# Kernel optimization log

Hardware: AMD Instinct MI355X
Metric: run time of the kernel (lower is better)

The kernel has to match this reference:

```python
import jax, jax.numpy as jnp
import numpy as np

B, T, D, DU, H = 2048, 100, 128, 128, 128  # batch, seq_len, emb_dim, user_emb_dim, hidden (=emb_dim)


def _mlp(x, layers, act):
    for W, b in layers:
        x = act(x @ W.T + b)
    return x


def setup_inputs() -> dict:
    key = jax.random.key(0)
    ks = iter(jax.random.split(key, 48))
    def p(shape, scale=0.05):
        return jax.random.normal(next(ks), shape, jnp.float32) * scale
    lengths = jax.random.randint(next(ks), (B,), 1, T + 1).astype(jnp.int32)
    mask = (jnp.arange(T)[None, :] < lengths[:, None]).astype(jnp.int32)
    inp = {
        'user_embedding': p((B, DU), 1.0),
        'item_historical_embedding': p((B, T, D), 1.0),
        'item_embedding': p((B, D), 1.0),
        'mask': mask,
        'sequential_length': lengths,
        'gru_Wih': p((3 * H, D)), 'gru_Whh': p((3 * H, H)),
        'gru_bih': p((3 * H,)), 'gru_bhh': p((3 * H,)),
        'aug_Wr': p((H, D + H)), 'aug_br': p((H,)),
        'aug_Wu': p((H, D + H)), 'aug_bu': p((H,)),
        'aug_Wh': p((H, D + H)), 'aug_bh': p((H,)),
    }
    att_dims = [4 * D, 80, 40, 1]
    ph_dims = [4 * D + DU, 200, 80, 1]
    for i, (di, do) in enumerate(zip(att_dims[:-1], att_dims[1:])):
        inp['att_W%d' % i] = p((do, di)); inp['att_b%d' % i] = p((do,))
    for i, (di, do) in enumerate(zip(ph_dims[:-1], ph_dims[1:])):
        inp['ph_W%d' % i] = p((do, di)); inp['ph_b%d' % i] = p((do,))
    return inp


def _forward(mask, sequential_length, user_embedding, item_historical_embedding, item_embedding,
             gru_Wih, gru_Whh, gru_bih, gru_bhh,
             att_W0, att_b0, att_W1, att_b1, att_W2, att_b2,
             aug_Wr, aug_br, aug_Wu, aug_bu, aug_Wh, aug_bh,
             ph_W0, ph_b0, ph_W1, ph_b1, ph_W2, ph_b2):
    fmask = mask.astype(jnp.float32)
    hist_sum = (item_historical_embedding * fmask[:, :, None]).sum(1)
    hist_sum = hist_sum / sequential_length[:, None].astype(jnp.float32)  # (B, D)

    # standard GRU over time (torch nn.GRU gate math) via lax.scan
    def gru_step(h, x_t):
        gi = x_t @ gru_Wih.T + gru_bih
        gh = h @ gru_Whh.T + gru_bhh
        i_r, i_z, i_n = jnp.split(gi, 3, axis=-1)
        h_r, h_z, h_n = jnp.split(gh, 3, axis=-1)
        r = jax.nn.sigmoid(i_r + h_r)
        z = jax.nn.sigmoid(i_z + h_z)
        n = jnp.tanh(i_n + r * h_n)
        h_new = (1.0 - z) * n + z * h
        return h_new, h_new
    h0 = jnp.zeros((item_historical_embedding.shape[0], H), jnp.float32)
    _, gru_seq = jax.lax.scan(gru_step, h0, jnp.swapaxes(item_historical_embedding, 0, 1))
    keys = jnp.swapaxes(gru_seq, 0, 1)  # (B, T, H)

    # DIN-style activation unit (all-ReLU MLP since act='relu'), masked softmax over time
    q = jnp.broadcast_to(item_embedding[:, None, :], keys.shape)
    feat = jnp.concatenate([keys, q, keys - q, q * keys], axis=-1)  # (B, T, 4H)
    score = _mlp(feat, [(att_W0, att_b0), (att_W1, att_b1), (att_W2, att_b2)], jax.nn.relu)
    score = jnp.where(mask[:, :, None] == 1, score, -jnp.inf)
    attn = jax.nn.softmax(score, axis=1)[..., 0]  # (B, T)
    # return_score=False in source: pooled context vector is (mis)used as attention scores
    pooled = jnp.einsum('bt,btd->bd', attn, keys)  # (B, H)

    # AUGRU; source indexes pooled[:, t] as per-step attention score (requires T <= H)
    att_seq = pooled.T[:T]  # (T, B)
    def augru_step(h, inp):
        x_t, a_t = inp
        ti = jnp.concatenate([h, x_t], axis=-1)
        r = jax.nn.sigmoid(ti @ aug_Wr.T + aug_br)
        u = jax.nn.sigmoid(ti @ aug_Wu.T + aug_bu)
        h_hat = jnp.tanh(jnp.concatenate([h * r, x_t], axis=-1) @ aug_Wh.T + aug_bh)
        u = a_t[:, None] * u
        h_new = (1.0 - u) * h + u * h_hat
        return h_new, h_new
    _, aug_seq = jax.lax.scan(augru_step, h0, (jnp.swapaxes(keys, 0, 1), att_seq))
    aug_out = jnp.swapaxes(aug_seq, 0, 1)  # (B, T, H)

    idx = (sequential_length - 1).astype(jnp.int32)[:, None, None]
    attention_feature = jnp.take_along_axis(aug_out, idx, axis=1)[:, 0, :]  # (B, H)

    comb = jnp.concatenate([user_embedding, item_embedding, hist_sum,
                            item_embedding * hist_sum, attention_feature], axis=1)
    # PredictHead: all layers sigmoid (source's i != len(dims)-1 is always True)
    scores = _mlp(comb, [(ph_W0, ph_b0), (ph_W1, ph_b1), (ph_W2, ph_b2)], jax.nn.sigmoid)
    return scores[:, 0]


def reference(user_embedding, item_historical_embedding, item_embedding, mask, sequential_length,
              gru_Wih, gru_Whh, gru_bih, gru_bhh,
              att_W0, att_b0, att_W1, att_b1, att_W2, att_b2,
              aug_Wr, aug_br, aug_Wu, aug_bu, aug_Wh, aug_bh,
              ph_W0, ph_b0, ph_W1, ph_b1, ph_W2, ph_b2):
    return _forward(mask, sequential_length, user_embedding, item_historical_embedding, item_embedding,
                    gru_Wih, gru_Whh, gru_bih, gru_bhh,
                    att_W0, att_b0, att_W1, att_b1, att_W2, att_b2,
                    aug_Wr, aug_br, aug_Wu, aug_bu, aug_Wh, aug_bh,
                    ph_W0, ph_b0, ph_W1, ph_b1, ph_W2, ph_b2)
```

## Files before the change

kernel.cpp:

```cpp
#include <hip/hip_runtime.h>
#include <math.h>

#define BB 2048
#define TT 100
#define DD 128
#define HH 128

typedef __attribute__((ext_vector_type(8))) short bf16x8;
typedef __attribute__((ext_vector_type(4))) float f32x4;

__device__ __forceinline__ float sigm(float x) {
    return __builtin_amdgcn_rcpf(1.f + __expf(-x));
}
__device__ __forceinline__ float tanh_fast(float x) {
    x = fminf(fmaxf(x, -15.f), 15.f);
    float e = __expf(2.f * x);
    return (e - 1.f) * __builtin_amdgcn_rcpf(e + 1.f);
}
__device__ __forceinline__ short f2bf(float f) {
    union { float f; unsigned u; } v; v.f = f;
    unsigned r = v.u + 0x7FFF + ((v.u >> 16) & 1);
    return (short)(r >> 16);
}
__device__ __forceinline__ float bf2f(ushort u) {
    union { unsigned u; float f; } v; v.u = ((unsigned)u) << 16;
    return v.f;
}

#define RD_A(buf, kk) (*(const bf16x8*)((const char*)(buf) + arow * 256 + (((kk) * 64 + akg * 16) ^ ((arow & 7) << 4))))
#define ST_A(buf, row, c, val) (*(short*)((char*)(buf) + (row) * 256 + (((c) * 2) ^ (((row) & 7) << 4))) = (val))

__global__ void k_prep(const float* __restrict__ attW0,
                       float* __restrict__ Wk, float* __restrict__ Wd, float* __restrict__ WqmC) {
    int i = blockIdx.x * 256 + threadIdx.x;
    if (i < 128 * 80) {
        int d = i / 80, j = i - d * 80;
        Wk[i]   = attW0[j * 512 + d] + attW0[j * 512 + 256 + d];
        Wd[i]   = attW0[j * 512 + 384 + d];
        WqmC[i] = attW0[j * 512 + 128 + d] - attW0[j * 512 + 256 + d];
    }
}

__global__ void k_pack(const float* __restrict__ Wih, const float* __restrict__ Whh,
                       const float* __restrict__ Wr, const float* __restrict__ Wu, const float* __restrict__ Wh,
                       const float* __restrict__ attW1,
                       const float* __restrict__ phW0, const float* __restrict__ phW1,
                       ushort* __restrict__ Pgru, ushort* __restrict__ Pa1, ushort* __restrict__ Pa2,
                       ushort* __restrict__ W1bf, ushort* __restrict__ W0h, ushort* __restrict__ W1h) {
    int n = blockIdx.x * 256 + threadIdx.x;
    if (n < 98304) {
        int tile = n >> 11, kt = (n >> 9) & 3, li = (n >> 3) & 63, e = n & 7;
        int k = kt * 32 + (li >> 4) * 8 + e;
        float s;
        if (tile < 24) { int j = tile * 16 + (li & 15); s = Wih[j * 128 + k]; }
        else           { int j = (tile - 24) * 16 + (li & 15); s = Whh[j * 128 + k]; }
        Pgru[n] = (ushort)f2bf(s);
    }
    if (n < 65536) {
        int tile = n >> 12, kt = (n >> 9) & 7, li = (n >> 3) & 63, e = n & 7;
        int k = kt * 32 + (li >> 4) * 8 + e;
        int jj = tile * 16 + (li & 15);
        float s = (jj < 128) ? Wr[jj * 256 + k] : Wu[(jj - 128) * 256 + k];
        Pa1[n] = (ushort)f2bf(s);
    }
    if (n < 32768) {
        int tile = n >> 12, kt = (n >> 9) & 7, li = (n >> 3) & 63, e = n & 7;
        int k = kt * 32 + (li >> 4) * 8 + e;
        int j = tile * 16 + (li & 15);
        Pa2[n] = (ushort)f2bf(Wh[j * 256 + k]);
    }
    if (n < 4608) {
        int g = n >> 9;
        int nt = g / 3, kt = g - nt * 3;
        int li = (n >> 3) & 63, e = n & 7;
        int k = kt * 32 + (li >> 4) * 8 + e;
        int j2 = nt * 16 + (li & 15);
        float s = (k < 80 && j2 < 40) ? attW1[j2 * 80 + k] : 0.f;
        W1bf[n] = (ushort)f2bf(s);
    }
    if (n < 133120) {
        int g = n >> 9;
        int nt = g / 20, kt = g - nt * 20;
        int li = (n >> 3) & 63, e = n & 7;
        int k = kt * 32 + (li >> 4) * 8 + e;
        int j = nt * 16 + (li & 15);
        W0h[n] = (ushort)f2bf((j < 200) ? phW0[j * 640 + k] : 0.f);
    }
    if (n < 17920) {
        int g = n >> 9;
        int nt = g / 7, kt = g - nt * 7;
        int li = (n >> 3) & 63, e = n & 7;
        int k = kt * 32 + (li >> 4) * 8 + e;
        int j = nt * 16 + (li & 15);
        W1h[n] = (ushort)f2bf((k < 200 && j < 80) ? phW1[j * 200 + k] : 0.f);
    }
}

__global__ void k_weffbf(const float* __restrict__ item, const float* __restrict__ Wk,
                         const float* __restrict__ Wd, const float* __restrict__ WqmC,
                         const float* __restrict__ attb0,
                         ushort* __restrict__ Weffbf, float* __restrict__ bias2) {
    int b = blockIdx.x, tid = threadIdx.x;
    __shared__ float q[128];
    if (tid < 128) q[tid] = item[b * 128 + tid];
    __syncthreads();
    ushort* Wb = Weffbf + (size_t)b * 10240;
    for (int idx = tid; idx < 10240; idx += 256) {
        int e = idx & 7, li = (idx >> 3) & 63, kt = (idx >> 9) & 3, nt = idx >> 11;
        int d = kt * 32 + (li >> 4) * 8 + e;
        int j = nt * 16 + (li & 15);
        Wb[idx] = (ushort)f2bf(Wk[d * 80 + j] + q[d] * Wd[d * 80 + j]);
    }
    if (tid < 80) {
        float s = attb0[tid];
        for (int d = 0; d < 128; ++d) s += q[d] * WqmC[d * 80 + tid];
        bias2[b * 80 + tid] = s;
    }
}

__global__ __launch_bounds__(512) void k_gru_mfma(const float* __restrict__ hist,
                                                  const ushort* __restrict__ Wp,
                                                  const float* __restrict__ bih, const float* __restrict__ bhh,
                                                  const int* __restrict__ len,
                                                  ushort* __restrict__ keysbf, float* __restrict__ hsum) {
    int tid = threadIdx.x;
    int lane = tid & 63, w = tid >> 6;
    int b0 = blockIdx.x * 8;

    __shared__ ushort xbf[2][16 * 128];
    __shared__ ushort hbf[2][16 * 128];
    __shared__ int    ln_s[8];

    for (int e = tid; e < 16 * 128; e += 512) { xbf[0][e] = 0; xbf[1][e] = 0; hbf[0][e] = 0; hbf[1][e] = 0; }
    if (tid < 8) ln_s[tid] = len[b0 + tid];

    const bf16x8* Wv = (const bf16x8*)Wp;
    bf16x8 bfx[3][4], bfh[3][4];
#pragma unroll
    for (int g = 0; g < 3; ++g)
#pragma unroll
        for (int kt = 0; kt < 4; ++kt) {
            bfx[g][kt] = Wv[((g * 8 + w) * 4 + kt) * 64 + lane];
            bfh[g][kt] = Wv[(((24 + g * 8 + w)) * 4 + kt) * 64 + lane];
        }

    int arow = lane & 15, akg = lane >> 4;
    int c = w * 16 + arow;
    float birq = bih[c] + bhh[c];
    float bizq = bih[128 + c] + bhh[128 + c];
    float bin  = bih[256 + c];
    float bqn  = bhh[256 + c];
    float hold[4] = {0.f, 0.f, 0.f, 0.f};

    int srow = tid >> 6, sd0 = (tid & 63) * 2;
    const float* hsrc = &hist[(size_t)(b0 + srow) * TT * DD + sd0];
    float2 v = *(const float2*)hsrc;
    __syncthreads();
    int Lrow = ln_s[srow];
    float sum0 = 0.f, sum1 = 0.f;
    {
        unsigned pv = (unsigned)(unsigned short)f2bf(v.x) | ((unsigned)(unsigned short)f2bf(v.y) << 16);
        *(unsigned*)((char*)xbf[0] + srow * 256 + ((sd0 * 2) ^ ((srow & 7) << 4))) = pv;
        if (0 < Lrow) { sum0 += v.x; sum1 += v.y; }
        if (TT > 1) v = *(const float2*)(hsrc + DD);
    }
    __syncthreads();

    f32x4 accr, accz, accnx;
    {
        bf16x8 af[4];
#pragma unroll
        for (int kt = 0; kt < 4; ++kt) af[kt] = RD_A(xbf[0], kt);
        accr = (f32x4){0.f,0.f,0.f,0.f}; accz = accr; accnx = accr;
#pragma unroll
        for (int kt = 0; kt < 4; ++kt) {
            accr  = __builtin_amdgcn_mfma_f32_16x16x32_bf16(af[kt], bfx[0][kt], accr, 0, 0, 0);
            accz  = __builtin_amdgcn_mfma_f32_16x16x32_bf16(af[kt], bfx[1][kt], accz, 0, 0, 0);
            accnx = __builtin_amdgcn_mfma_f32_16x16x32_bf16(af[kt], bfx[2][kt], accnx, 0, 0, 0);
        }
    }

    int p = 0, q = 0;
    for (int t = 0; t < TT; ++t) {
        if (t + 1 < TT) {
            unsigned pv = (unsigned)(unsigned short)f2bf(v.x) | ((unsigned)(unsigned short)f2bf(v.y) << 16);
            *(unsigned*)((char*)xbf[p ^ 1] + srow * 256 + ((sd0 * 2) ^ ((srow & 7) << 4))) = pv;
            if (t + 1 < Lrow) { sum0 += v.x; sum1 += v.y; }
            if (t + 2 < TT) v = *(const float2*)(hsrc + (size_t)(t + 2) * DD);
        }

        bf16x8 ah[4];
#pragma unroll
        for (int kt = 0; kt < 4; ++kt) ah[kt] = RD_A(hbf[q], kt);
        f32x4 accnh = {0.f, 0.f, 0.f, 0.f};
#pragma unroll
        for (int kt = 0; kt < 4; ++kt) {
            accr  = __builtin_amdgcn_mfma_f32_16x16x32_bf16(ah[kt], bfh[0][kt], accr, 0, 0, 0);
            accz  = __builtin_amdgcn_mfma_f32_16x16x32_bf16(ah[kt], bfh[1][kt], accz, 0, 0, 0);
            accnh = __builtin_amdgcn_mfma_f32_16x16x32_bf16(ah[kt], bfh[2][kt], accnh, 0, 0, 0);
        }

        ushort* hw = (ushort*)hbf[q ^ 1];
#pragma unroll
        for (int i = 0; i < 4; ++i) {
            float r = sigm(accr[i] + birq);
            float z = sigm(accz[i] + bizq);
            float nn = tanh_fast(accnx[i] + bin + r * (accnh[i] + bqn));
            float hnew = (1.f - z) * nn + z * hold[i];
            hold[i] = hnew;
            if (akg < 2) {
                int row = akg * 4 + i;
                short hb16 = f2bf(hnew);
                ST_A(hw, row, c, hb16);
                keysbf[((size_t)(b0 + row) * TT + t) * HH + c] = (ushort)hb16;
            }
        }
        __syncthreads();

        if (t + 1 < TT) {
            bf16x8 af[4];
#pragma unroll
            for (int kt = 0; kt < 4; ++kt) af[kt] = RD_A(xbf[p ^ 1], kt);
            f32x4 ar = {0.f,0.f,0.f,0.f}, az = ar, an = ar;
#pragma unroll
            for (int kt = 0; kt < 4; ++kt) {
                ar = __builtin_amdgcn_mfma_f32_16x16x32_bf16(af[kt], bfx[0][kt], ar, 0, 0, 0);
                az = __builtin_amdgcn_mfma_f32_16x16x32_bf16(af[kt], bfx[1][kt], az, 0, 0, 0);
                an = __builtin_amdgcn_mfma_f32_16x16x32_bf16(af[kt], bfx[2][kt], an, 0, 0, 0);
            }
            accr = ar; accz = az; accnx = an;
        }
        p ^= 1; q ^= 1;
    }

    hsum[(b0 + srow) * 128 + sd0]     = sum0 / (float)Lrow;
    hsum[(b0 + srow) * 128 + sd0 + 1] = sum1 / (float)Lrow;
}

__global__ __launch_bounds__(512) void k_attnsoft(const ushort* __restrict__ keysbf,
                                                  const ushort* __restrict__ Weffbf,
                                                  const float* __restrict__ bias2,
                                                  const ushort* __restrict__ W1bf,
                                                  const float* __restrict__ attb1, const float* __restrict__ attW2,
                                                  const float* __restrict__ attb2,
                                                  const int* __restrict__ len,
                                                  float* __restrict__ pooled) {
    int tid = threadIdx.x;
    int lane = tid & 63, w = tid >> 6;
    int b = blockIdx.x;

    __shared__ ushort kbf[112 * 128];
    __shared__ ushort scbf[112 * 96];
    __shared__ float  bias2s[80];
    __shared__ float  b1s[48];
    __shared__ float  W2s[48];
    __shared__ float  attn_s[128];
    __shared__ float  red[128];
    __shared__ float  pred[512];

    bf16x8 bfrag0[5][4];
    bf16x8 bfrag1[3][3];
    if (w < 7) {
        const bf16x8* Wb = (const bf16x8*)(Weffbf + (size_t)b * 10240);
#pragma unroll
        for (int nt = 0; nt < 5; ++nt)
#pragma unroll
            for (int kt = 0; kt < 4; ++kt)
                bfrag0[nt][kt] = Wb[(nt * 4 + kt) * 64 + lane];
#pragma unroll
        for (int nt = 0; nt < 3; ++nt)
#pragma unroll
            for (int kt = 0; kt < 3; ++kt)
                bfrag1[nt][kt] = ((const bf16x8*)W1bf)[(nt * 3 + kt) * 64 + lane];
    }

    const ushort* ksrc = keysbf + (size_t)b * TT * 128;
    for (int e = tid; e < 3584; e += 512) {
        int row = e >> 5, c4 = e & 31;
        uint2 pv;
        if (row < TT) pv = *(const uint2*)(ksrc + row * 128 + c4 * 4);
        else { pv.x = 0; pv.y = 0; }
        *(uint2*)((char*)kbf + row * 256 + ((c4 * 8) ^ ((row & 7) << 4))) = pv;
    }
    for (int e = tid; e < 1792; e += 512) {
        int row = e >> 4, c = 80 + (e & 15);
        *(ushort*)((char*)scbf + row * 192 + ((c * 2) ^ ((row & 7) << 4))) = 0;
    }
    if (tid < 80) bias2s[tid] = bias2[b * 80 + tid];
    if (tid < 48) {
        b1s[tid] = (tid < 40) ? attb1[tid] : 0.f;
        W2s[tid] = (tid < 40) ? attW2[tid] : 0.f;
    }
    __syncthreads();

    if (w < 7) {
        int arow = lane & 15, akg = lane >> 4;
        int row = w * 16 + arow;
        bf16x8 af[4];
#pragma unroll
        for (int kt = 0; kt < 4; ++kt)
            af[kt] = *(const bf16x8*)((const char*)kbf + row * 256 + (((kt * 64 + akg * 16)) ^ ((row & 7) << 4)));
#pragma unroll
        for (int nt = 0; nt < 5; ++nt) {
            f32x4 acc = {0.f, 0.f, 0.f, 0.f};
#pragma unroll
            for (int kt = 0; kt < 4; ++kt)
                acc = __builtin_amdgcn_mfma_f32_16x16x32_bf16(af[kt], bfrag0[nt][kt], acc, 0, 0, 0);
            int col = nt * 16 + arow;
            float bcol = bias2s[col];
#pragma unroll
            for (int i = 0; i < 4; ++i) {
                int r2 = w * 16 + akg * 4 + i;
                float vsc = fmaxf(acc[i] + bcol, 0.f);
                *(short*)((char*)scbf + r2 * 192 + ((col * 2) ^ ((r2 & 7) << 4))) = f2bf(vsc);
            }
        }
    }
    __syncthreads();

    if (w < 7) {
        int arow = lane & 15, akg = lane >> 4;
        int row = w * 16 + arow;
        bf16x8 a1[3];
#pragma unroll
        for (int kt = 0; kt < 3; ++kt)
            a1[kt] = *(const bf16x8*)((const char*)scbf + row * 192 + (((kt * 64 + akg * 16)) ^ ((row & 7) << 4)));
        float pi[4] = {0.f, 0.f, 0.f, 0.f};
#pragma unroll
        for (int nt = 0; nt < 3; ++nt) {
            f32x4 acc = {0.f, 0.f, 0.f, 0.f};
#pragma unroll
            for (int kt = 0; kt < 3; ++kt)
                acc = __builtin_amdgcn_mfma_f32_16x16x32_bf16(a1[kt], bfrag1[nt][kt], acc, 0, 0, 0);
            int col = nt * 16 + arow;
            float wb = W2s[col], bb1 = b1s[col];
#pragma unroll
            for (int i = 0; i < 4; ++i)
                pi[i] += fmaxf(acc[i] + bb1, 0.f) * wb;
        }
#pragma unroll
        for (int off = 1; off < 16; off <<= 1)
#pragma unroll
            for (int i = 0; i < 4; ++i)
                pi[i] += __shfl_xor(pi[i], off);
        if ((lane & 15) == 0) {
            float b2 = attb2[0];
#pragma unroll
            for (int i = 0; i < 4; ++i) {
                int t = w * 16 + akg * 4 + i;
                if (t < 128) attn_s[t] = fmaxf(pi[i] + b2, 0.f);
            }
        }
    }
    __syncthreads();

    int L = len[b];
    if (tid < 128) red[tid] = (tid < L) ? attn_s[tid] : -INFINITY;
    __syncthreads();
    for (int o = 64; o >= 1; o >>= 1) { if (tid < o) red[tid] = fmaxf(red[tid], red[tid + o]); __syncthreads(); }
    float mx = red[0];
    __syncthreads();
    if (tid < 128) {
        float e = (tid < L) ? __expf(attn_s[tid] - mx) : 0.f;
        attn_s[tid] = e; red[tid] = e;
    }
    __syncthreads();
    for (int o = 64; o >= 1; o >>= 1) { if (tid < o) red[tid] += red[tid + o]; __syncthreads(); }
    float inv = __builtin_amdgcn_rcpf(red[0]);
    {
        int d = tid & 127, qd = tid >> 7;
        float p = 0.f;
        for (int t2 = qd; t2 < L; t2 += 4) {
            ushort kv = *(const ushort*)((const char*)kbf + t2 * 256 + ((d * 2) ^ ((t2 & 7) << 4)));
            p += attn_s[t2] * bf2f(kv);
        }
        pred[tid] = p;
    }
    __syncthreads();
    if (tid < 128)
        pooled[b * 128 + tid] = (pred[tid] + pred[128 + tid] + pred[256 + tid] + pred[384 + tid]) * inv;
}

__global__ __launch_bounds__(512) void k_augru_mfma(const ushort* __restrict__ keysbf,
                                                    const float* __restrict__ pooled,
                                                    const int* __restrict__ len,
                                                    const ushort* __restrict__ Wp1, const ushort* __restrict__ Wp2,
                                                    const float* __restrict__ br, const float* __restrict__ bu,
                                                    const float* __restrict__ bh,
                                                    float* __restrict__ att_feat) {
    int tid = threadIdx.x;
    int lane = tid & 63, w = tid >> 6;
    int b0 = blockIdx.x * 8;

    __shared__ ushort hbf[16 * 128], rhbf[16 * 128];
    __shared__ ushort xbf[2][16 * 128];
    __shared__ float as_[16];
    __shared__ int ln_s[8];

    for (int e = tid; e < 16 * 128; e += 512) { hbf[e] = 0; rhbf[e] = 0; xbf[0][e] = 0; xbf[1][e] = 0; }
    if (tid < 16) as_[tid] = 0.f;
    if (tid < 8) ln_s[tid] = len[b0 + tid];

    const bf16x8* W1v = (const bf16x8*)Wp1;
    const bf16x8* W2v = (const bf16x8*)Wp2;
    bf16x8 b1r[8], b1u[8], b2[8];
#pragma unroll
    for (int kt = 0; kt < 8; ++kt) {
        b1r[kt] = W1v[(w * 8 + kt) * 64 + lane];
        b1u[kt] = W1v[((8 + w) * 8 + kt) * 64 + lane];
        b2[kt]  = W2v[(w * 8 + kt) * 64 + lane];
    }

    int arow = lane & 15, akg = lane >> 4;
    int c = w * 16 + arow;
    float brc = br[c], buc = bu[c], bhc = bh[c];
    float hold[4] = {0.f, 0.f, 0.f, 0.f};

    int srow = tid >> 6, sd0 = (tid & 63) * 2;
    const ushort* xsrc = &keysbf[(size_t)(b0 + srow) * TT * HH + sd0];
    unsigned v0 = *(const unsigned*)xsrc;
    float areg = (tid < 8) ? pooled[(b0 + tid) * HH + 0] : 0.f;
    __syncthreads();
    *(unsigned*)((char*)xbf[0] + srow * 256 + ((sd0 * 2) ^ ((srow & 7) << 4))) = v0;
    if (tid < 8) as_[tid] = areg;
    unsigned vnext = (TT > 1) ? *(const unsigned*)(xsrc + (size_t)1 * HH) : 0u;
    float aregn = (tid < 8 && TT > 1) ? pooled[(b0 + tid) * HH + 1] : 0.f;
    __syncthreads();

    f32x4 accr = {0.f,0.f,0.f,0.f}, accu = {0.f,0.f,0.f,0.f}, acchx = {0.f,0.f,0.f,0.f};
    {
        bf16x8 af[4];
#pragma unroll
        for (int kt = 0; kt < 4; ++kt) af[kt] = RD_A(xbf[0], kt);
#pragma unroll
        for (int kt = 0; kt < 4; ++kt) {
            accr  = __builtin_amdgcn_mfma_f32_16x16x32_bf16(af[kt], b1r[4 + kt], accr, 0, 0, 0);
            accu  = __builtin_amdgcn_mfma_f32_16x16x32_bf16(af[kt], b1u[4 + kt], accu, 0, 0, 0);
            acchx = __builtin_amdgcn_mfma_f32_16x16x32_bf16(af[kt], b2[4 + kt], acchx, 0, 0, 0);
        }
    }

    int p = 0;
    for (int t = 0; t < TT; ++t) {
        if (t + 1 < TT) {
            *(unsigned*)((char*)xbf[p ^ 1] + srow * 256 + ((sd0 * 2) ^ ((srow & 7) << 4))) = vnext;
            if (t + 2 < TT) vnext = *(const unsigned*)(xsrc + (size_t)(t + 2) * HH);
        }

        bf16x8 ah[4];
#pragma unroll
        for (int kt = 0; kt < 4; ++kt) ah[kt] = RD_A(hbf, kt);
#pragma unroll
        for (int kt = 0; kt < 4; ++kt) {
            accr = __builtin_amdgcn_mfma_f32_16x16x32_bf16(ah[kt], b1r[kt], accr, 0, 0, 0);
            accu = __builtin_amdgcn_mfma_f32_16x16x32_bf16(ah[kt], b1u[kt], accu, 0, 0, 0);
        }

        float u_reg[4];
#pragma unroll
        for (int i = 0; i < 4; ++i) {
            float r = sigm(accr[i] + brc);
            u_reg[i] = as_[akg * 4 + i] * sigm(accu[i] + buc);
            if (akg < 2) ST_A(rhbf, akg * 4 + i, c, f2bf(r * hold[i]));
        }
        __syncthreads();

        bf16x8 arh[4];
#pragma unroll
        for (int kt = 0; kt < 4; ++kt) arh[kt] = RD_A(rhbf, kt);
        f32x4 acch = acchx;
        f32x4 accr2 = {0.f,0.f,0.f,0.f}, accu2 = {0.f,0.f,0.f,0.f}, acchx2 = {0.f,0.f,0.f,0.f};
#pragma unroll
        for (int kt = 0; kt < 4; ++kt)
            acch = __builtin_amdgcn_mfma_f32_16x16x32_bf16(arh[kt], b2[kt], acch, 0, 0, 0);
        if (t + 1 < TT) {
            bf16x8 axn[4];
#pragma unroll
            for (int kt = 0; kt < 4; ++kt) axn[kt] = RD_A(xbf[p ^ 1], kt);
#pragma unroll
            for (int kt = 0; kt < 4; ++kt) {
                accr2  = __builtin_amdgcn_mfma_f32_16x16x32_bf16(axn[kt], b1r[4 + kt], accr2, 0, 0, 0);
                accu2  = __builtin_amdgcn_mfma_f32_16x16x32_bf16(axn[kt], b1u[4 + kt], accu2, 0, 0, 0);
                acchx2 = __builtin_amdgcn_mfma_f32_16x16x32_bf16(axn[kt], b2[4 + kt], acchx2, 0, 0, 0);
            }
        }

#pragma unroll
        for (int i = 0; i < 4; ++i) {
            float hhat = tanh_fast(acch[i] + bhc);
            float hnew = (1.f - u_reg[i]) * hold[i] + u_reg[i] * hhat;
            hold[i] = hnew;
            if (akg < 2) {
                int row = akg * 4 + i;
                ST_A(hbf, row, c, f2bf(hnew));
                if (t == ln_s[row] - 1) att_feat[(b0 + row) * HH + c] = hnew;
            }
        }
        if (tid < 8) as_[tid] = aregn;
        if (tid < 8 && t + 2 < TT) aregn = pooled[(b0 + tid) * HH + t + 2];
        __syncthreads();

        accr = accr2; accu = accu2; acchx = acchx2;
        p ^= 1;
    }
}

__global__ __launch_bounds__(64) void k_head(const float* __restrict__ user, const float* __restrict__ item,
                                             const float* __restrict__ hsum, const float* __restrict__ attf,
                                             const ushort* __restrict__ W0h, const ushort* __restrict__ W1h,
                                             const float* __restrict__ phb0, const float* __restrict__ phb1,
                                             const float* __restrict__ phW2, const float* __restrict__ phb2,
                                             float* __restrict__ out) {
    int lane = threadIdx.x;
    int b0 = blockIdx.x * 16;
    __shared__ ushort xb[16 * 128];
    __shared__ ushort h1b[16 * 256];

    for (int e = lane; e < 4096; e += 64) h1b[e] = 0;

    int arow = lane & 15, akg = lane >> 4;
    f32x4 acc0[13];
#pragma unroll
    for (int nt = 0; nt < 13; ++nt) acc0[nt] = (f32x4){0.f, 0.f, 0.f, 0.f};

    for (int c = 0; c < 5; ++c) {
        for (int idx = lane; idx < 1024; idx += 64) {
            int row = idx >> 6, c2 = (idx & 63) * 2;
            int g = (b0 + row) * 128 + c2;
            float2 v;
            if (c == 0) v = *(const float2*)&user[g];
            else if (c == 1) v = *(const float2*)&item[g];
            else if (c == 2) v = *(const float2*)&hsum[g];
            else if (c == 3) { float2 a = *(const float2*)&item[g]; float2 h = *(const float2*)&hsum[g];
                               v.x = a.x * h.x; v.y = a.y * h.y; }
            else v = *(const float2*)&attf[g];
            unsigned pv = (unsigned)(unsigned short)f2bf(v.x) | ((unsigned)(unsigned short)f2bf(v.y) << 16);
            *(unsigned*)((char*)xb + row * 256 + ((c2 * 2) ^ ((row & 7) << 4))) = pv;
        }
        __syncthreads();
        bf16x8 af[4];
#pragma unroll
        for (int kt = 0; kt < 4; ++kt)
            af[kt] = *(const bf16x8*)((const char*)xb + arow * 256 + ((kt * 64 + akg * 16) ^ ((arow & 7) << 4)));
#pragma unroll
        for (int nt = 0; nt < 13; ++nt) {
#pragma unroll
            for (int kt = 0; kt < 4; ++kt) {
                int ktg = c * 4 + kt;
                bf16x8 bf = ((const bf16x8*)W0h)[(nt * 20 + ktg) * 64 + lane];
                acc0[nt] = __builtin_amdgcn_mfma_f32_16x16x32_bf16(af[kt], bf, acc0[nt], 0, 0, 0);
            }
        }
        __syncthreads();
    }

#pragma unroll
    for (int nt = 0; nt < 13; ++nt) {
        int col = nt * 16 + arow;
        if (col < 200) {
            float bb = phb0[col];
#pragma unroll
            for (int i = 0; i < 4; ++i) {
                int r2 = akg * 4 + i;
                *(short*)((char*)h1b + r2 * 512 + ((col * 2) ^ ((r2 & 7) << 4))) = f2bf(sigm(acc0[nt][i] + bb));
            }
        }
    }
    __syncthreads();

    bf16x8 a1[7];
#pragma unroll
    for (int kt = 0; kt < 7; ++kt)
        a1[kt] = *(const bf16x8*)((const char*)h1b + arow * 512 + ((kt * 64 + akg * 16) ^ ((arow & 7) << 4)));
    float pi[4] = {0.f, 0.f, 0.f, 0.f};
#pragma unroll
    for (int nt = 0; nt < 5; ++nt) {
        f32x4 acc = {0.f, 0.f, 0.f, 0.f};
#pragma unroll
        for (int kt = 0; kt < 7; ++kt)
            acc = __builtin_amdgcn_mfma_f32_16x16x32_bf16(a1[kt], ((const bf16x8*)W1h)[(nt * 7 + kt) * 64 + lane], acc, 0, 0, 0);
        int col = nt * 16 + arow;
        float b1 = phb1[col], w2v = phW2[col];
#pragma unroll
        for (int i = 0; i < 4; ++i)
            pi[i] += sigm(acc[i] + b1) * w2v;
    }
#pragma unroll
    for (int off = 1; off < 16; off <<= 1)
#pragma unroll
        for (int i = 0; i < 4; ++i)
            pi[i] += __shfl_xor(pi[i], off);
    if (arow == 0) {
        float b2 = phb2[0];
#pragma unroll
        for (int i = 0; i < 4; ++i)
            out[b0 + akg * 4 + i] = sigm(pi[i] + b2);
    }
}

extern "C" void kernel_launch(void* const* d_in, const int* in_sizes, int n_in,
                              void* d_out, int out_size, void* d_ws, size_t ws_size,
                              hipStream_t stream) {
    const float* user = (const float*)d_in[0];
    const float* hist = (const float*)d_in[1];
    const float* item = (const float*)d_in[2];
    const int* len = (const int*)d_in[4];
    const float* gWih = (const float*)d_in[5];
    const float* gWhh = (const float*)d_in[6];
    const float* gbih = (const float*)d_in[7];
    const float* gbhh = (const float*)d_in[8];
    const float* aWr = (const float*)d_in[9];
    const float* abr = (const float*)d_in[10];
    const float* aWu = (const float*)d_in[11];
    const float* abu = (const float*)d_in[12];
    const float* aWh = (const float*)d_in[13];
    const float* abh = (const float*)d_in[14];
    const float* attW0 = (const float*)d_in[15];
    const float* attb0 = (const float*)d_in[16];
    const float* attW1 = (const float*)d_in[17];
    const float* attb1 = (const float*)d_in[18];
    const float* attW2 = (const float*)d_in[19];
    const float* attb2 = (const float*)d_in[20];
    const float* phW0 = (const float*)d_in[21];
    const float* phb0 = (const float*)d_in[22];
    const float* phW1 = (const float*)d_in[23];
    const float* phb1 = (const float*)d_in[24];
    const float* phW2 = (const float*)d_in[25];
    const float* phb2 = (const float*)d_in[26];

    char* ws = (char*)d_ws;
    size_t off = 0;
    auto alloc = [&](size_t bytes) { char* p = ws + off; off += (bytes + 255) & ~(size_t)255; return p; };
    ushort* keysbf  = (ushort*)alloc((size_t)BB * TT * HH * 2);
    ushort* Weffbf  = (ushort*)alloc((size_t)BB * 10240 * 2);
    float* pooled   = (float*)alloc((size_t)BB * HH * 4);
    float* hsum     = (float*)alloc((size_t)BB * DD * 4);
    float* attf     = (float*)alloc((size_t)BB * HH * 4);
    float* Wk       = (float*)alloc(128 * 80 * 4);
    float* Wd       = (float*)alloc(128 * 80 * 4);
    float* WqmC     = (float*)alloc(128 * 80 * 4);
    float* bias2    = (float*)alloc((size_t)BB * 80 * 4);
    ushort* Pgru    = (ushort*)alloc(98304 * 2);
    ushort* Pa1     = (ushort*)alloc(65536 * 2);
    ushort* Pa2     = (ushort*)alloc(32768 * 2);
    ushort* W1bf    = (ushort*)alloc(4608 * 2);
    ushort* W0h     = (ushort*)alloc(133120 * 2);
    ushort* W1h     = (ushort*)alloc(17920 * 2);
    (void)in_sizes; (void)n_in; (void)out_size; (void)ws_size;

    k_prep<<<40, 256, 0, stream>>>(attW0, Wk, Wd, WqmC);
    k_pack<<<520, 256, 0, stream>>>(gWih, gWhh, aWr, aWu, aWh, attW1, phW0, phW1,
                                    Pgru, Pa1, Pa2, W1bf, W0h, W1h);
    k_weffbf<<<BB, 256, 0, stream>>>(item, Wk, Wd, WqmC, attb0, Weffbf, bias2);
    k_gru_mfma<<<256, 512, 0, stream>>>(hist, Pgru, gbih, gbhh, len, keysbf, hsum);
    k_attnsoft<<<BB, 512, 0, stream>>>(keysbf, Weffbf, bias2, W1bf, attb1, attW2, attb2, len, pooled);
    k_augru_mfma<<<256, 512, 0, stream>>>(keysbf, pooled, len, Pa1, Pa2, abr, abu, abh, attf);
    k_head<<<128, 64, 0, stream>>>(user, item, hsum, attf, W0h, W1h, phb0, phb1, phW2, phb2, (float*)d_out);
}
```

Before: 401.2 us.

## Halve AUGRU block to 4 waves, each computing two 16-column MFMA tiles

The AUGRU kernel now runs with 256 threads per block instead of 512. Each wave owns two 16-column output tiles, so the B-fragment weight registers double and every wave issues twice as many MFMAs per step. The goal is to cut the cost of the two block-wide barriers in each of the 100 serial timesteps by syncing fewer waves. Hidden-state writes to LDS are also packed into 32-bit stores using a lane shuffle. The trade-off is higher register pressure, since 48 bf16x8 fragments stay resident, and less MFMA parallelism per CU on a latency-bound recurrence.

```diff
diff --git a/kernel.cpp b/kernel.cpp
--- a/kernel.cpp
+++ b/kernel.cpp
@@ -381,13 +381,13 @@
         pooled[b * 128 + tid] = (pred[tid] + pred[128 + tid] + pred[256 + tid] + pred[384 + tid]) * inv;
 }
 
-__global__ __launch_bounds__(512) void k_augru_mfma(const ushort* __restrict__ keysbf,
-                                                    const float* __restrict__ pooled,
-                                                    const int* __restrict__ len,
-                                                    const ushort* __restrict__ Wp1, const ushort* __restrict__ Wp2,
-                                                    const float* __restrict__ br, const float* __restrict__ bu,
-                                                    const float* __restrict__ bh,
-                                                    float* __restrict__ att_feat) {
+__global__ __launch_bounds__(256, 1) void k_augru_mfma(const ushort* __restrict__ keysbf,
+                                                       const float* __restrict__ pooled,
+                                                       const int* __restrict__ len,
+                                                       const ushort* __restrict__ Wp1, const ushort* __restrict__ Wp2,
+                                                       const float* __restrict__ br, const float* __restrict__ bu,
+                                                       const float* __restrict__ bh,
+                                                       float* __restrict__ att_feat) {
     int tid = threadIdx.x;
     int lane = tid & 63, w = tid >> 6;
     int b0 = blockIdx.x * 8;
@@ -397,110 +397,152 @@
     __shared__ float as_[16];
     __shared__ int ln_s[8];
 
-    for (int e = tid; e < 16 * 128; e += 512) { hbf[e] = 0; rhbf[e] = 0; xbf[0][e] = 0; xbf[1][e] = 0; }
+    for (int e = tid; e < 16 * 128; e += 256) { hbf[e] = 0; rhbf[e] = 0; xbf[0][e] = 0; xbf[1][e] = 0; }
     if (tid < 16) as_[tid] = 0.f;
     if (tid < 8) ln_s[tid] = len[b0 + tid];
 
     const bf16x8* W1v = (const bf16x8*)Wp1;
     const bf16x8* W2v = (const bf16x8*)Wp2;
-    bf16x8 b1r[8], b1u[8], b2[8];
-#pragma unroll
-    for (int kt = 0; kt < 8; ++kt) {
-        b1r[kt] = W1v[(w * 8 + kt) * 64 + lane];
-        b1u[kt] = W1v[((8 + w) * 8 + kt) * 64 + lane];
-        b2[kt]  = W2v[(w * 8 + kt) * 64 + lane];
-    }
+    bf16x8 b1r[2][8], b1u[2][8], b2[2][8];
+#pragma unroll
+    for (int f = 0; f < 2; ++f)
+#pragma unroll
+        for (int kt = 0; kt < 8; ++kt) {
+            b1r[f][kt] = W1v[((2 * w + f) * 8 + kt) * 64 + lane];
+            b1u[f][kt] = W1v[((8 + 2 * w + f) * 8 + kt) * 64 + lane];
+            b2[f][kt]  = W2v[((2 * w + f) * 8 + kt) * 64 + lane];
+        }
 
     int arow = lane & 15, akg = lane >> 4;
-    int c = w * 16 + arow;
-    float brc = br[c], buc = bu[c], bhc = bh[c];
-    float hold[4] = {0.f, 0.f, 0.f, 0.f};
+    int c0 = 32 * w + arow, c1 = c0 + 16;
+    float brc[2] = {br[c0], br[c1]};
+    float buc[2] = {bu[c0], bu[c1]};
+    float bhc[2] = {bh[c0], bh[c1]};
+    float hold[2][4] = {{0.f,0.f,0.f,0.f},{0.f,0.f,0.f,0.f}};
 
     int srow = tid >> 6, sd0 = (tid & 63) * 2;
-    const ushort* xsrc = &keysbf[(size_t)(b0 + srow) * TT * HH + sd0];
-    unsigned v0 = *(const unsigned*)xsrc;
+    const ushort* xsrcA = &keysbf[(size_t)(b0 + srow) * TT * HH + sd0];
+    const ushort* xsrcB = &keysbf[(size_t)(b0 + srow + 4) * TT * HH + sd0];
+    unsigned vA = *(const unsigned*)xsrcA, vB = *(const unsigned*)xsrcB;
     float areg = (tid < 8) ? pooled[(b0 + tid) * HH + 0] : 0.f;
     __syncthreads();
-    *(unsigned*)((char*)xbf[0] + srow * 256 + ((sd0 * 2) ^ ((srow & 7) << 4))) = v0;
+    *(unsigned*)((char*)xbf[0] + srow * 256 + ((sd0 * 2) ^ ((srow & 7) << 4))) = vA;
+    *(unsigned*)((char*)xbf[0] + (srow + 4) * 256 + ((sd0 * 2) ^ (((srow + 4) & 7) << 4))) = vB;
     if (tid < 8) as_[tid] = areg;
-    unsigned vnext = (TT > 1) ? *(const unsigned*)(xsrc + (size_t)1 * HH) : 0u;
+    unsigned vnA = (TT > 1) ? *(const unsigned*)(xsrcA + HH) : 0u;
+    unsigned vnB = (TT > 1) ? *(const unsigned*)(xsrcB + HH) : 0u;
     float aregn = (tid < 8 && TT > 1) ? pooled[(b0 + tid) * HH + 1] : 0.f;
     __syncthreads();
 
-    f32x4 accr = {0.f,0.f,0.f,0.f}, accu = {0.f,0.f,0.f,0.f}, acchx = {0.f,0.f,0.f,0.f};
+    f32x4 accr[2], accu[2], acchx[2];
     {
         bf16x8 af[4];
 #pragma unroll
         for (int kt = 0; kt < 4; ++kt) af[kt] = RD_A(xbf[0], kt);
 #pragma unroll
-        for (int kt = 0; kt < 4; ++kt) {
-            accr  = __builtin_amdgcn_mfma_f32_16x16x32_bf16(af[kt], b1r[4 + kt], accr, 0, 0, 0);
-            accu  = __builtin_amdgcn_mfma_f32_16x16x32_bf16(af[kt], b1u[4 + kt], accu, 0, 0, 0);
-            acchx = __builtin_amdgcn_mfma_f32_16x16x32_bf16(af[kt], b2[4 + kt], acchx, 0, 0, 0);
+        for (int f = 0; f < 2; ++f) {
+            accr[f] = (f32x4){0.f,0.f,0.f,0.f}; accu[f] = accr[f]; acchx[f] = accr[f];
+#pragma unroll
+            for (int kt = 0; kt < 4; ++kt) {
+                accr[f]  = __builtin_amdgcn_mfma_f32_16x16x32_bf16(af[kt], b1r[f][4 + kt], accr[f], 0, 0, 0);
+                accu[f]  = __builtin_amdgcn_mfma_f32_16x16x32_bf16(af[kt], b1u[f][4 + kt], accu[f], 0, 0, 0);
+                acchx[f] = __builtin_amdgcn_mfma_f32_16x16x32_bf16(af[kt], b2[f][4 + kt], acchx[f], 0, 0, 0);
+            }
         }
     }
 
     int p = 0;
     for (int t = 0; t < TT; ++t) {
         if (t + 1 < TT) {
-            *(unsigned*)((char*)xbf[p ^ 1] + srow * 256 + ((sd0 * 2) ^ ((srow & 7) << 4))) = vnext;
-            if (t + 2 < TT) vnext = *(const unsigned*)(xsrc + (size_t)(t + 2) * HH);
+            *(unsigned*)((char*)xbf[p ^ 1] + srow * 256 + ((sd0 * 2) ^ ((srow & 7) << 4))) = vnA;
+            *(unsigned*)((char*)xbf[p ^ 1] + (srow + 4) * 256 + ((sd0 * 2) ^ (((srow + 4) & 7) << 4))) = vnB;
+            if (t + 2 < TT) {
+                vnA = *(const unsigned*)(xsrcA + (size_t)(t + 2) * HH);
+                vnB = *(const unsigned*)(xsrcB + (size_t)(t + 2) * HH);
+            }
         }
 
         bf16x8 ah[4];
 #pragma unroll
         for (int kt = 0; kt < 4; ++kt) ah[kt] = RD_A(hbf, kt);
 #pragma unroll
-        for (int kt = 0; kt < 4; ++kt) {
-            accr = __builtin_amdgcn_mfma_f32_16x16x32_bf16(ah[kt], b1r[kt], accr, 0, 0, 0);
-            accu = __builtin_amdgcn_mfma_f32_16x16x32_bf16(ah[kt], b1u[kt], accu, 0, 0, 0);
-        }
-
-        float u_reg[4];
-#pragma unroll
-        for (int i = 0; i < 4; ++i) {
-            float r = sigm(accr[i] + brc);
-            u_reg[i] = as_[akg * 4 + i] * sigm(accu[i] + buc);
-            if (akg < 2) ST_A(rhbf, akg * 4 + i, c, f2bf(r * hold[i]));
+        for (int f = 0; f < 2; ++f)
+#pragma unroll
+            for (int kt = 0; kt < 4; ++kt) {
+                accr[f] = __builtin_amdgcn_mfma_f32_16x16x32_bf16(ah[kt], b1r[f][kt], accr[f], 0, 0, 0);
+                accu[f] = __builtin_amdgcn_mfma_f32_16x16x32_bf16(ah[kt], b1u[f][kt], accu[f], 0, 0, 0);
+            }
+
+        float u_reg[2][4];
+#pragma unroll
+        for (int f = 0; f < 2; ++f) {
+            int cc = (f == 0) ? c0 : c1;
+#pragma unroll
+            for (int i = 0; i < 4; ++i) {
+                float r = sigm(accr[f][i] + brc[f]);
+                u_reg[f][i] = as_[akg * 4 + i] * sigm(accu[f][i] + buc[f]);
+                unsigned mine = (unsigned)(unsigned short)f2bf(r * hold[f][i]);
+                unsigned other = __shfl_xor(mine, 1);
+                if ((arow & 1) == 0 && akg < 2) {
+                    int row = akg * 4 + i;
+                    *(unsigned*)((char*)rhbf + row * 256 + (((cc * 2)) ^ ((row & 7) << 4))) = mine | (other << 16);
+                }
+            }
         }
         __syncthreads();
 
         bf16x8 arh[4];
 #pragma unroll
         for (int kt = 0; kt < 4; ++kt) arh[kt] = RD_A(rhbf, kt);
-        f32x4 acch = acchx;
-        f32x4 accr2 = {0.f,0.f,0.f,0.f}, accu2 = {0.f,0.f,0.f,0.f}, acchx2 = {0.f,0.f,0.f,0.f};
-#pragma unroll
-        for (int kt = 0; kt < 4; ++kt)
-            acch = __builtin_amdgcn_mfma_f32_16x16x32_bf16(arh[kt], b2[kt], acch, 0, 0, 0);
+        f32x4 acch[2];
+        f32x4 accr2[2], accu2[2], acchx2[2];
+#pragma unroll
+        for (int f = 0; f < 2; ++f) {
+            acch[f] = acchx[f];
+#pragma unroll
+            for (int kt = 0; kt < 4; ++kt)
+                acch[f] = __builtin_amdgcn_mfma_f32_16x16x32_bf16(arh[kt], b2[f][kt], acch[f], 0, 0, 0);
+        }
         if (t + 1 < TT) {
             bf16x8 axn[4];
 #pragma unroll
             for (int kt = 0; kt < 4; ++kt) axn[kt] = RD_A(xbf[p ^ 1], kt);
 #pragma unroll
-            for (int kt = 0; kt < 4; ++kt) {
-                accr2  = __builtin_amdgcn_mfma_f32_16x16x32_bf16(axn[kt], b1r[4 + kt], accr2, 0, 0, 0);
-                accu2  = __builtin_amdgcn_mfma_f32_16x16x32_bf16(axn[kt], b1u[4 + kt], accu2, 0, 0, 0);
-                acchx2 = __builtin_amdgcn_mfma_f32_16x16x32_bf16(axn[kt], b2[4 + kt], acchx2, 0, 0, 0);
-            }
-        }
-
-#pragma unroll
-        for (int i = 0; i < 4; ++i) {
-            float hhat = tanh_fast(acch[i] + bhc);
-            float hnew = (1.f - u_reg[i]) * hold[i] + u_reg[i] * hhat;
-            hold[i] = hnew;
-            if (akg < 2) {
-                int row = akg * 4 + i;
-                ST_A(hbf, row, c, f2bf(hnew));
-                if (t == ln_s[row] - 1) att_feat[(b0 + row) * HH + c] = hnew;
+            for (int f = 0; f < 2; ++f) {
+                accr2[f] = (f32x4){0.f,0.f,0.f,0.f}; accu2[f] = accr2[f]; acchx2[f] = accr2[f];
+#pragma unroll
+                for (int kt = 0; kt < 4; ++kt) {
+                    accr2[f]  = __builtin_amdgcn_mfma_f32_16x16x32_bf16(axn[kt], b1r[f][4 + kt], accr2[f], 0, 0, 0);
+                    accu2[f]  = __builtin_amdgcn_mfma_f32_16x16x32_bf16(axn[kt], b1u[f][4 + kt], accu2[f], 0, 0, 0);
+                    acchx2[f] = __builtin_amdgcn_mfma_f32_16x16x32_bf16(axn[kt], b2[f][4 + kt], acchx2[f], 0, 0, 0);
+                }
+            }
+        }
+
+#pragma unroll
+        for (int f = 0; f < 2; ++f) {
+            int cc = (f == 0) ? c0 : c1;
+#pragma unroll
+            for (int i = 0; i < 4; ++i) {
+                float hhat = tanh_fast(acch[f][i] + bhc[f]);
+                float hnew = (1.f - u_reg[f][i]) * hold[f][i] + u_reg[f][i] * hhat;
+                hold[f][i] = hnew;
+                unsigned mine = (unsigned)(unsigned short)f2bf(hnew);
+                unsigned other = __shfl_xor(mine, 1);
+                if (akg < 2) {
+                    int row = akg * 4 + i;
+                    if ((arow & 1) == 0)
+                        *(unsigned*)((char*)hbf + row * 256 + (((cc * 2)) ^ ((row & 7) << 4))) = mine | (other << 16);
+                    if (t == ln_s[row] - 1) att_feat[(b0 + row) * HH + cc] = hnew;
+                }
             }
         }
         if (tid < 8) as_[tid] = aregn;
         if (tid < 8 && t + 2 < TT) aregn = pooled[(b0 + tid) * HH + t + 2];
         __syncthreads();
 
-        accr = accr2; accu = accu2; acchx = acchx2;
+#pragma unroll
+        for (int f = 0; f < 2; ++f) { accr[f] = accr2[f]; accu[f] = accu2[f]; acchx[f] = acchx2[f]; }
         p ^= 1;
     }
 }
@@ -654,6 +696,6 @@
     k_weffbf<<<BB, 256, 0, stream>>>(item, Wk, Wd, WqmC, attb0, Weffbf, bias2);
     k_gru_mfma<<<256, 512, 0, stream>>>(hist, Pgru, gbih, gbhh, len, keysbf, hsum);
     k_attnsoft<<<BB, 512, 0, stream>>>(keysbf, Weffbf, bias2, W1bf, attb1, attW2, attb2, len, pooled);
-    k_augru_mfma<<<256, 512, 0, stream>>>(keysbf, pooled, len, Pa1, Pa2, abr, abu, abh, attf);
+    k_augru_mfma<<<256, 256, 0, stream>>>(keysbf, pooled, len, Pa1, Pa2, abr, abu, abh, attf);
     k_head<<<128, 64, 0, stream>>>(user, item, hsum, attf, W0h, W1h, phb0, phb1, phW2, phb2, (float*)d_out);
 }
```

Result: slower. 528.4 us (+31.7%).
